# Performance work log

Hardware: AMD Instinct MI355X
Metric: run time of the kernel (lower is better)

The kernel has to match this reference:

```python
import jax, jax.numpy as jnp
import numpy as np

B, S, D, H = 4, 2048, 1024, 16
DEPTH = D // H


def setup_inputs() -> dict:
    key = jax.random.key(0)
    ks = jax.random.split(key, 12)
    q = jax.random.normal(ks[0], (B, S, D), dtype=jnp.float32)
    k = jax.random.normal(ks[1], (B, S, D), dtype=jnp.float32)
    v = jax.random.normal(ks[2], (B, S, D), dtype=jnp.float32)
    # causal mask: 1.0 where attention is disallowed (upper triangle), per `mask * -1e9`
    mask = 1.0 - jnp.tril(jnp.ones((S, S), dtype=jnp.float32))
    mask = mask[None, None, :, :]  # [1,1,S,S] broadcastable over batch/heads
    scale = 1.0 / np.sqrt(D)
    Wq = jax.random.normal(ks[3], (D, D), dtype=jnp.float32) * scale
    Wk = jax.random.normal(ks[4], (D, D), dtype=jnp.float32) * scale
    Wv = jax.random.normal(ks[5], (D, D), dtype=jnp.float32) * scale
    Wo = jax.random.normal(ks[6], (D, D), dtype=jnp.float32) * scale
    bq = jnp.zeros((D,), jnp.float32)
    bk = jnp.zeros((D,), jnp.float32)
    bv = jnp.zeros((D,), jnp.float32)
    bo = jnp.zeros((D,), jnp.float32)
    return {"query": q, "key": k, "value": v, "mask": mask,
            "Wq": Wq, "bq": bq, "Wk": Wk, "bk": bk,
            "Wv": Wv, "bv": bv, "Wo": Wo, "bo": bo}


def _split_heads(x):
    # [B, S, D] -> [B, H, S, depth]
    b, s, _ = x.shape
    return x.reshape(b, s, H, DEPTH).transpose(0, 2, 1, 3)


def reference(query, key, value, mask, Wq, bq, Wk, bk, Wv, bv, Wo, bo):
    q = _split_heads(query @ Wq + bq)   # [B,H,S,depth]
    k = _split_heads(key @ Wk + bk)
    v = _split_heads(value @ Wv + bv)
    scores = jnp.einsum('bhqd,bhkd->bhqk', q, k) / jnp.sqrt(
        jnp.asarray(DEPTH, q.dtype))
    scores = scores + mask * (-1e9)
    attn = jax.nn.softmax(scores, axis=-1)
    out = jnp.einsum('bhqk,bhkd->bhqd', attn, v)   # [B,H,S,depth]
    out = out.transpose(0, 2, 1, 3).reshape(query.shape[0], -1, H * DEPTH)
    return out @ Wo + bo
```

## Files before the change

kernel.cpp:

```cpp
#include <hip/hip_runtime.h>

#define Bsz 4
#define SEQ 2048
#define DIM 1024
#define NH 16
#define HD 64

typedef float  f32x4  __attribute__((ext_vector_type(4)));
typedef __bf16 bf16x8 __attribute__((ext_vector_type(8)));
typedef __bf16 bf16x4 __attribute__((ext_vector_type(4)));
typedef short  s16x4  __attribute__((ext_vector_type(4)));

__device__ __forceinline__ f32x4 mfma16(bf16x8 a, bf16x8 b, f32x4 c) {
    return __builtin_amdgcn_mfma_f32_16x16x32_bf16(a, b, c, 0, 0, 0);
}
__device__ __forceinline__ f32x4 mfma16k16(bf16x4 a, bf16x4 b, f32x4 c) {
#if defined(__has_builtin) && __has_builtin(__builtin_amdgcn_mfma_f32_16x16x16bf16_1k)
    return __builtin_amdgcn_mfma_f32_16x16x16bf16_1k(
        __builtin_bit_cast(s16x4, a), __builtin_bit_cast(s16x4, b), c, 0, 0, 0);
#else
    asm volatile("s_nop 2\n\tv_mfma_f32_16x16x16_bf16 %0, %1, %2, %0\n\ts_nop 7\n\ts_nop 7"
                 : "+v"(c) : "v"(a), "v"(b));
    return c;
#endif
}

#define GLD_LDS16(gsrc, ldst)                                                        \
    __builtin_amdgcn_global_load_lds(                                                \
        (const __attribute__((address_space(1))) void*)(gsrc),                       \
        (__attribute__((address_space(3))) void*)(ldst), 16, 0, 0)

__global__ __launch_bounds__(256) void cvt_kernel(
    const float* __restrict__ x0, const float* __restrict__ x1,
    const float* __restrict__ x2,
    __bf16* __restrict__ o0, __bf16* __restrict__ o1, __bf16* __restrict__ o2)
{
    int z = blockIdx.y;
    const float* X = (z == 0) ? x0 : (z == 1) ? x1 : x2;
    __bf16*      O = (z == 0) ? o0 : (z == 1) ? o1 : o2;
    size_t i = ((size_t)blockIdx.x * 256 + threadIdx.x) * 8;
    f32x4 a = *(const f32x4*)(X + i);
    f32x4 b = *(const f32x4*)(X + i + 4);
    bf16x8 r;
#pragma unroll
    for (int j = 0; j < 4; j++) { r[j] = (__bf16)a[j]; r[4 + j] = (__bf16)b[j]; }
    *(bf16x8*)(O + i) = r;
}

__global__ __launch_bounds__(256) void wt_kernel(
    const float* __restrict__ Wq, const float* __restrict__ Wk,
    const float* __restrict__ Wv, const float* __restrict__ Wo,
    __bf16* __restrict__ wt)
{
    __shared__ float tile[64][65];
    int z = blockIdx.z;
    const float* W = (z == 0) ? Wq : (z == 1) ? Wk : (z == 2) ? Wv : Wo;
    __bf16* out = wt + (size_t)z * DIM * DIM;
    int kb = blockIdx.x * 64, nb = blockIdx.y * 64;
    int t = threadIdx.x;
    int cidx = t & 63, ridx = t >> 6;
#pragma unroll
    for (int i = 0; i < 16; i++) {
        int r = ridx + i * 4;
        tile[r][cidx] = W[(size_t)(kb + r) * DIM + nb + cidx];
    }
    __syncthreads();
#pragma unroll
    for (int i = 0; i < 16; i++) {
        int r = ridx + i * 4;
        out[(size_t)(nb + r) * DIM + kb + cidx] = (__bf16)tile[cidx][r];
    }
}

__global__ __launch_bounds__(256, 2) void gemm_proj(
    const __bf16* __restrict__ Xq, const __bf16* __restrict__ Xk,
    const __bf16* __restrict__ Xv, const __bf16* __restrict__ wt,
    const float* __restrict__ bq, const float* __restrict__ bk,
    const float* __restrict__ bv,
    __bf16* __restrict__ oq, __bf16* __restrict__ ok, __bf16* __restrict__ ovT)
{
    int z = blockIdx.z;
    const __bf16* X    = (z == 0) ? Xq : (z == 1) ? Xk : Xv;
    const float*  bias = (z == 0) ? bq : (z == 1) ? bk : bv;
    const __bf16* Bt   = wt + (size_t)z * DIM * DIM;

    __shared__ __align__(16) char smem[32768];
    __bf16* const Ab = (__bf16*)smem;
    __bf16* const Bb = (__bf16*)(smem + 16384);

    int m0 = blockIdx.x * 128, n0 = blockIdx.y * 128;
    int tid = threadIdx.x, lane = tid & 63, w = tid >> 6;
    int c = lane & 15, g = lane >> 4;
    int wm = (w >> 1) * 64, wn = (w & 1) * 64;

    f32x4 acc[4][4] = {};

    int srow = (w * 2) * 16 + (lane >> 2);
    int scol = (lane & 3) * 8;
    const __bf16* aptr0 = X + (size_t)(m0 + srow) * DIM + scol;
    const __bf16* aptr1 = aptr0 + (size_t)16 * DIM;
    const __bf16* bptr0 = Bt + (size_t)(n0 + srow) * DIM + scol;
    const __bf16* bptr1 = bptr0 + (size_t)16 * DIM;
    int so0 = (w * 2) * 512;
    int so1 = (w * 2 + 1) * 512;

    GLD_LDS16(aptr0, Ab + so0);
    GLD_LDS16(aptr1, Ab + so1);
    GLD_LDS16(bptr0, Bb + so0);
    GLD_LDS16(bptr1, Bb + so1);
    __syncthreads();

    int cur = 0;
    for (int kt = 0; kt < 32; ++kt) {
        int nxt = kt + 1;
        int nb = cur ^ 1;
        if (nxt < 32) {
            int k0 = nxt * 32;
            GLD_LDS16(aptr0 + k0, Ab + nb * 4096 + so0);
            GLD_LDS16(aptr1 + k0, Ab + nb * 4096 + so1);
            GLD_LDS16(bptr0 + k0, Bb + nb * 4096 + so0);
            GLD_LDS16(bptr1 + k0, Bb + nb * 4096 + so1);
        }
        bf16x8 af[4], bf[4];
#pragma unroll
        for (int mf = 0; mf < 4; mf++)
            af[mf] = *(bf16x8*)&Ab[cur * 4096 + (wm + mf * 16 + c) * 32 + g * 8];
#pragma unroll
        for (int nf = 0; nf < 4; nf++)
            bf[nf] = *(bf16x8*)&Bb[cur * 4096 + (wn + nf * 16 + c) * 32 + g * 8];
#pragma unroll
        for (int mf = 0; mf < 4; mf++)
#pragma unroll
            for (int nf = 0; nf < 4; nf++)
                acc[mf][nf] = mfma16(af[mf], bf[nf], acc[mf][nf]);
        __syncthreads();
        cur = nb;
    }

    if (z == 2) {
        __bf16* T = (__bf16*)smem + (size_t)w * 2304;
        int h = (n0 + wn) >> 6;
        int bb = m0 >> 11;
        int s_base = (m0 & (SEQ - 1)) + wm;
        int dd = lane >> 2;
        int ss = (lane & 3) * 8;
        size_t obase = ((size_t)(bb * NH + h) * HD) * SEQ;
#pragma unroll
        for (int half = 0; half < 2; half++) {
#pragma unroll
            for (int mh = 0; mh < 2; mh++) {
                int mf = half * 2 + mh;
#pragma unroll
                for (int nf = 0; nf < 4; nf++) {
                    int col = n0 + wn + nf * 16 + c;
                    int d = nf * 16 + c;
                    float bval = bias[col];
                    bf16x4 pk;
#pragma unroll
                    for (int r = 0; r < 4; r++) pk[r] = (__bf16)(acc[mf][nf][r] + bval);
                    *(bf16x4*)&T[d * 36 + mh * 16 + g * 4] = pk;
                }
            }
#pragma unroll
            for (int dgrp = 0; dgrp < 4; dgrp++) {
                int d = dgrp * 16 + dd;
                bf16x8 vv = *(bf16x8*)&T[d * 36 + ss];
                *(bf16x8*)&ovT[obase + (size_t)d * SEQ + s_base + half * 32 + ss] = vv;
            }
        }
    } else {
        __bf16* Out = (z == 0) ? oq : ok;
#pragma unroll
        for (int nf = 0; nf < 4; nf++) {
            int col = n0 + wn + nf * 16 + c;
            float bval = bias[col];
#pragma unroll
            for (int mf = 0; mf < 4; mf++) {
                int row = m0 + wm + mf * 16 + g * 4;
#pragma unroll
                for (int r = 0; r < 4; r++)
                    Out[(size_t)(row + r) * DIM + col] = (__bf16)(acc[mf][nf][r] + bval);
            }
        }
    }
}

__global__ __launch_bounds__(256, 2) void gemm_proj_f32(
    const float* __restrict__ Xq, const float* __restrict__ Xk,
    const float* __restrict__ Xv, const __bf16* __restrict__ wt,
    const float* __restrict__ bq, const float* __restrict__ bk,
    const float* __restrict__ bv,
    __bf16* __restrict__ oq, __bf16* __restrict__ ok, __bf16* __restrict__ ovT)
{
    int z = blockIdx.z;
    const float*  X    = (z == 0) ? Xq : (z == 1) ? Xk : Xv;
    const float*  bias = (z == 0) ? bq : (z == 1) ? bk : bv;
    const __bf16* Bt   = wt + (size_t)z * DIM * DIM;

    __shared__ __align__(16) char smem[36864];
    __bf16* const Ab = (__bf16*)smem;
    __bf16* const Bb = (__bf16*)(smem + 16384);

    int m0 = blockIdx.x * 128, n0 = blockIdx.y * 128;
    int tid = threadIdx.x, lane = tid & 63, w = tid >> 6;
    int c = lane & 15, g = lane >> 4;
    int wm = (w >> 1) * 64, wn = (w & 1) * 64;

    f32x4 acc[4][4] = {};

    int ar = tid >> 1, ah = tid & 1;
    const float* aptr = X + (size_t)(m0 + ar) * DIM + ah * 16;
    int awo = ar * 32 + ah * 16;

    int brow0 = (w * 2) * 16 + (lane >> 2);
    int bcol  = (lane & 3) * 8;
    const __bf16* bptr0 = Bt + (size_t)(n0 + brow0) * DIM + bcol;
    const __bf16* bptr1 = bptr0 + (size_t)16 * DIM;
    int bwo0 = (w * 2) * 512;
    int bwo1 = (w * 2 + 1) * 512;

    {
        f32x4 f0 = *(const f32x4*)(aptr);
        f32x4 f1 = *(const f32x4*)(aptr + 4);
        f32x4 f2 = *(const f32x4*)(aptr + 8);
        f32x4 f3 = *(const f32x4*)(aptr + 12);
        GLD_LDS16(bptr0, Bb + bwo0);
        GLD_LDS16(bptr1, Bb + bwo1);
        bf16x8 b0, b1;
#pragma unroll
        for (int j = 0; j < 4; j++) {
            b0[j] = (__bf16)f0[j]; b0[4 + j] = (__bf16)f1[j];
            b1[j] = (__bf16)f2[j]; b1[4 + j] = (__bf16)f3[j];
        }
        *(bf16x8*)(Ab + awo)     = b0;
        *(bf16x8*)(Ab + awo + 8) = b1;
    }
    __syncthreads();

    int cur = 0;
    for (int kt = 0; kt < 32; ++kt) {
        int nxt = kt + 1;
        int nb = cur ^ 1;
        f32x4 f0, f1, f2, f3;
        if (nxt < 32) {
            const float* ap = aptr + nxt * 32;
            f0 = *(const f32x4*)(ap);
            f1 = *(const f32x4*)(ap + 4);
            f2 = *(const f32x4*)(ap + 8);
            f3 = *(const f32x4*)(ap + 12);
            GLD_LDS16(bptr0 + nxt * 32, Bb + nb * 4096 + bwo0);
            GLD_LDS16(bptr1 + nxt * 32, Bb + nb * 4096 + bwo1);
        }
        bf16x8 af[4], bf[4];
#pragma unroll
        for (int mf = 0; mf < 4; mf++)
            af[mf] = *(bf16x8*)&Ab[cur * 4096 + (wm + mf * 16 + c) * 32 + g * 8];
#pragma unroll
        for (int nf = 0; nf < 4; nf++)
            bf[nf] = *(bf16x8*)&Bb[cur * 4096 + (wn + nf * 16 + c) * 32 + g * 8];
#pragma unroll
        for (int mf = 0; mf < 4; mf++)
#pragma unroll
            for (int nf = 0; nf < 4; nf++)
                acc[mf][nf] = mfma16(af[mf], bf[nf], acc[mf][nf]);
        if (nxt < 32) {
            bf16x8 b0, b1;
#pragma unroll
            for (int j = 0; j < 4; j++) {
                b0[j] = (__bf16)f0[j]; b0[4 + j] = (__bf16)f1[j];
                b1[j] = (__bf16)f2[j]; b1[4 + j] = (__bf16)f3[j];
            }
            *(bf16x8*)(Ab + nb * 4096 + awo)     = b0;
            *(bf16x8*)(Ab + nb * 4096 + awo + 8) = b1;
        }
        __syncthreads();
        cur = nb;
    }

    if (z == 2) {
        __bf16* T = (__bf16*)smem + (size_t)w * 4608;
#pragma unroll
        for (int nf = 0; nf < 4; nf++) {
            int col = n0 + wn + nf * 16 + c;
            int d = nf * 16 + c;
            float bval = bias[col];
#pragma unroll
            for (int mf = 0; mf < 4; mf++) {
                int sl = mf * 16 + g * 4;
                bf16x4 pk;
#pragma unroll
                for (int r = 0; r < 4; r++) pk[r] = (__bf16)(acc[mf][nf][r] + bval);
                *(bf16x4*)&T[d * 72 + sl] = pk;
            }
        }
        int h = (n0 + wn) >> 6;
        int bb = m0 >> 11;
        int s_base = (m0 & (SEQ - 1)) + wm;
        int dd = lane >> 2;
        int ss = (lane & 3) * 8;
        size_t obase = ((size_t)(bb * NH + h) * HD) * SEQ;
#pragma unroll
        for (int dgrp = 0; dgrp < 4; dgrp++)
#pragma unroll
            for (int half = 0; half < 2; half++) {
                int d = dgrp * 16 + dd;
                int s = half * 32 + ss;
                bf16x8 vv = *(bf16x8*)&T[d * 72 + s];
                *(bf16x8*)&ovT[obase + (size_t)d * SEQ + s_base + s] = vv;
            }
    } else {
        __bf16* Out = (z == 0) ? oq : ok;
#pragma unroll
        for (int nf = 0; nf < 4; nf++) {
            int col = n0 + wn + nf * 16 + c;
            float bval = bias[col];
#pragma unroll
            for (int mf = 0; mf < 4; mf++) {
                int row = m0 + wm + mf * 16 + g * 4;
#pragma unroll
                for (int r = 0; r < 4; r++)
                    Out[(size_t)(row + r) * DIM + col] = (__bf16)(acc[mf][nf][r] + bval);
            }
        }
    }
}

#define QSCALE 0.180336880f

__global__ __launch_bounds__(256, 2) void fa_kernel(
    const __bf16* __restrict__ qp, const __bf16* __restrict__ kp,
    const __bf16* __restrict__ vpT, __bf16* __restrict__ op)
{
    int bz = blockIdx.x;
    int bh = bz & 63;
    int b = bh >> 4, h = bh & 15;
    int qt = 31 - (bz >> 6);
    int q0 = qt * 64;

    int tid = threadIdx.x, lane = tid & 63, w = tid >> 6;
    int c = lane & 15, g = lane >> 4;

    __shared__ __bf16 Kbuf[64 * 64];
    __shared__ __bf16 Vbuf[64 * 64];

    const int qb = q0 + w * 16;
    const int qg = qb + c;

    bf16x8 qf[2];
    {
        const __bf16* qbase = qp + (size_t)(b * SEQ + qg) * DIM + h * HD;
#pragma unroll
        for (int kc = 0; kc < 2; kc++) {
            bf16x8 raw = *(const bf16x8*)(qbase + kc * 32 + g * 8);
            bf16x8 sc;
#pragma unroll
            for (int j = 0; j < 8; j++) sc[j] = (__bf16)((float)raw[j] * QSCALE);
            qf[kc] = sc;
        }
    }

    f32x4 acc[4] = {};
    float m_run = -1e30f;
    float l_run = 0.f;

    int r8 = tid >> 3, c8 = tid & 7;
    int sch = c8 ^ (r8 & 7);
    const __bf16* kbase = kp  + (size_t)(b * SEQ + r8) * DIM + h * HD + sch * 8;
    const __bf16* vbase = vpT + ((size_t)(b * NH + h) * HD + r8) * SEQ + sch * 8;
    __bf16* kdst0 = Kbuf + w * 512;
    __bf16* kdst1 = Kbuf + 2048 + w * 512;
    __bf16* vdst0 = Vbuf + w * 512;
    __bf16* vdst1 = Vbuf + 2048 + w * 512;

    int vb4[4];
#pragma unroll
    for (int mkey = 0; mkey < 4; mkey++)
        vb4[mkey] = c * 64 + (((2 * mkey + (g >> 1)) ^ (c & 7)) * 8) + (g & 1) * 4;

    int ktmax = qt + 1;
    for (int kt = 0; kt < ktmax; ++kt) {
        GLD_LDS16(kbase + (size_t)kt * 64 * DIM, kdst0);
        GLD_LDS16(kbase + (size_t)(kt * 64 + 32) * DIM, kdst1);
        GLD_LDS16(vbase + kt * 64, vdst0);
        GLD_LDS16(vbase + kt * 64 + (size_t)32 * SEQ, vdst1);
        __syncthreads();

        int kb0 = kt * 64;

        f32x4 s[4] = {};
#pragma unroll
        for (int kc = 0; kc < 2; kc++) {
            bf16x8 kf[4];
#pragma unroll
            for (int mkey = 0; mkey < 4; mkey++)
                kf[mkey] = *(bf16x8*)&Kbuf[(mkey * 16 + c) * 64 + (((kc * 4 + g) ^ (c & 7)) * 8)];
#pragma unroll
            for (int mkey = 0; mkey < 4; mkey++)
                s[mkey] = mfma16(kf[mkey], qf[kc], s[mkey]);
        }

        if (kb0 + 63 > qg) {
#pragma unroll
            for (int mkey = 0; mkey < 4; mkey++)
#pragma unroll
                for (int r2 = 0; r2 < 4; r2++)
                    if (kb0 + mkey * 16 + g * 4 + r2 > qg) s[mkey][r2] = -1e30f;
        }

        float pm0 = fmaxf(fmaxf(s[0][0], s[0][1]), fmaxf(s[0][2], s[0][3]));
        float pm1 = fmaxf(fmaxf(s[1][0], s[1][1]), fmaxf(s[1][2], s[1][3]));
        float pm2 = fmaxf(fmaxf(s[2][0], s[2][1]), fmaxf(s[2][2], s[2][3]));
        float pm3 = fmaxf(fmaxf(s[3][0], s[3][1]), fmaxf(s[3][2], s[3][3]));
        float pm = fmaxf(fmaxf(pm0, pm1), fmaxf(pm2, pm3));
        pm = fmaxf(pm, __shfl_xor(pm, 16));
        pm = fmaxf(pm, __shfl_xor(pm, 32));
        if (!__all(pm <= m_run + 8.f)) {
            float mn = fmaxf(m_run, pm);
            float scl = exp2f(m_run - mn);
            l_run *= scl;
#pragma unroll
            for (int nf = 0; nf < 4; nf++) acc[nf] *= scl;
            m_run = mn;
        }
        float rs = 0.f;
        bf16x4 pf[4];
#pragma unroll
        for (int mkey = 0; mkey < 4; mkey++) {
            bf16x4 pk;
#pragma unroll
            for (int r2 = 0; r2 < 4; r2++) {
                float p = exp2f(s[mkey][r2] - m_run);
                rs += p;
                pk[r2] = (__bf16)p;
            }
            pf[mkey] = pk;
        }
        rs += __shfl_xor(rs, 16);
        rs += __shfl_xor(rs, 32);
        l_run += rs;

#pragma unroll
        for (int mkey = 0; mkey < 4; mkey++) {
#pragma unroll
            for (int nf = 0; nf < 4; nf++) {
                bf16x4 vf = *(bf16x4*)&Vbuf[vb4[mkey] + nf * 1024];
                acc[nf] = mfma16k16(vf, pf[mkey], acc[nf]);
            }
        }
        __syncthreads();
    }

    {
        float inv = 1.f / l_run;
        __bf16* obase = op + (size_t)(b * SEQ + qg) * DIM + h * HD + g * 4;
#pragma unroll
        for (int nf = 0; nf < 4; nf++) {
            bf16x4 pk;
#pragma unroll
            for (int r2 = 0; r2 < 4; r2++) pk[r2] = (__bf16)(acc[nf][r2] * inv);
            *(bf16x4*)(obase + nf * 16) = pk;
        }
    }
}

__global__ __launch_bounds__(256, 2) void gemm_out(
    const __bf16* __restrict__ Ain, const __bf16* __restrict__ wt,
    const float* __restrict__ bias, float* __restrict__ Out)
{
    const __bf16* Bt = wt + (size_t)3 * DIM * DIM;

    __shared__ __bf16 Ab[2][4096];
    __shared__ __bf16 Bb[2][4096];

    int m0 = blockIdx.x * 128, n0 = blockIdx.y * 128;
    int tid = threadIdx.x, lane = tid & 63, w = tid >> 6;
    int c = lane & 15, g = lane >> 4;
    int wm = (w >> 1) * 64, wn = (w & 1) * 64;

    f32x4 acc[4][4] = {};

    int srow = (w * 2) * 16 + (lane >> 2);
    int scol = (lane & 3) * 8;
    const __bf16* aptr0 = Ain + (size_t)(m0 + srow) * DIM + scol;
    const __bf16* aptr1 = aptr0 + (size_t)16 * DIM;
    const __bf16* bptr0 = Bt + (size_t)(n0 + srow) * DIM + scol;
    const __bf16* bptr1 = bptr0 + (size_t)16 * DIM;
    int so0 = (w * 2) * 512;
    int so1 = (w * 2 + 1) * 512;

    GLD_LDS16(aptr0, Ab[0] + so0);
    GLD_LDS16(aptr1, Ab[0] + so1);
    GLD_LDS16(bptr0, Bb[0] + so0);
    GLD_LDS16(bptr1, Bb[0] + so1);
    __syncthreads();

    int cur = 0;
    for (int kt = 0; kt < 32; ++kt) {
        int nxt = kt + 1;
        int nb = cur ^ 1;
        if (nxt < 32) {
            int k0 = nxt * 32;
            GLD_LDS16(aptr0 + k0, Ab[nb] + so0);
            GLD_LDS16(aptr1 + k0, Ab[nb] + so1);
            GLD_LDS16(bptr0 + k0, Bb[nb] + so0);
            GLD_LDS16(bptr1 + k0, Bb[nb] + so1);
        }
        bf16x8 af[4], bf[4];
#pragma unroll
        for (int mf = 0; mf < 4; mf++)
            af[mf] = *(bf16x8*)&Ab[cur][(wm + mf * 16 + c) * 32 + g * 8];
#pragma unroll
        for (int nf = 0; nf < 4; nf++)
            bf[nf] = *(bf16x8*)&Bb[cur][(wn + nf * 16 + c) * 32 + g * 8];
#pragma unroll
        for (int mf = 0; mf < 4; mf++)
#pragma unroll
            for (int nf = 0; nf < 4; nf++)
                acc[mf][nf] = mfma16(af[mf], bf[nf], acc[mf][nf]);
        __syncthreads();
        cur = nb;
    }

#pragma unroll
    for (int nf = 0; nf < 4; nf++) {
        int col = n0 + wn + nf * 16 + c;
        float bval = bias[col];
#pragma unroll
        for (int mf = 0; mf < 4; mf++) {
            int row = m0 + wm + mf * 16 + g * 4;
#pragma unroll
            for (int r = 0; r < 4; r++)
                Out[(size_t)(row + r) * DIM + col] = acc[mf][nf][r] + bval;
        }
    }
}

extern "C" void kernel_launch(void* const* d_in, const int* in_sizes, int n_in,
                              void* d_out, int out_size, void* d_ws, size_t ws_size,
                              hipStream_t stream)
{
    const float* q  = (const float*)d_in[0];
    const float* k  = (const float*)d_in[1];
    const float* v  = (const float*)d_in[2];
    const float* Wq = (const float*)d_in[4];
    const float* bq = (const float*)d_in[5];
    const float* Wk = (const float*)d_in[6];
    const float* bk = (const float*)d_in[7];
    const float* Wv = (const float*)d_in[8];
    const float* bv = (const float*)d_in[9];
    const float* Wo = (const float*)d_in[10];
    const float* bo = (const float*)d_in[11];

    char* ws = (char*)d_ws;
    __bf16* wt  = (__bf16*)ws;
    __bf16* qp  = (__bf16*)(ws + (size_t)(8u  << 20));
    __bf16* kp  = (__bf16*)(ws + (size_t)(24u << 20));
    __bf16* vpT = (__bf16*)(ws + (size_t)(40u << 20));
    __bf16* ao  = (__bf16*)(ws + (size_t)(56u << 20));
    __bf16* xq  = (__bf16*)(ws + (size_t)(72u << 20));
    __bf16* xk  = (__bf16*)(ws + (size_t)(88u << 20));
    __bf16* xv  = (__bf16*)(ws + (size_t)(104u << 20));

    wt_kernel<<<dim3(16, 16, 4), 256, 0, stream>>>(Wq, Wk, Wv, Wo, wt);
    if (ws_size >= ((size_t)120u << 20)) {
        cvt_kernel<<<dim3(4096, 3), 256, 0, stream>>>(q, k, v, xq, xk, xv);
        gemm_proj<<<dim3(64, 8, 3), 256, 0, stream>>>(xq, xk, xv, wt, bq, bk, bv, qp, kp, vpT);
    } else {
        gemm_proj_f32<<<dim3(64, 8, 3), 256, 0, stream>>>(q, k, v, wt, bq, bk, bv, qp, kp, vpT);
    }
    fa_kernel<<<dim3(2048), 256, 0, stream>>>(qp, kp, vpT, ao);
    gemm_out<<<dim3(64, 8), 256, 0, stream>>>(ao, wt, bo, (float*)d_out);

    (void)in_sizes; (void)n_in; (void)out_size;
}
```

Before: 196.2 us.

## Double-buffer K/V tiles in LDS and prefetch the next tile during compute

K and V shared-memory buffers are doubled. The next 64-key tile is issued as a global-to-LDS load before the current tile's QK and PV MFMAs run, which drops the top-of-loop barrier that waited on each load. The row-max reduction is rewritten as a linear chain suited to three-input max instructions, and the row-sum is split into four independent accumulators. LDS use per block doubles, which could limit occupancy, and correctness relies on the end-of-loop barrier waiting for the outstanding async loads.

```diff
diff --git a/kernel.cpp b/kernel.cpp
--- a/kernel.cpp
+++ b/kernel.cpp
@@ -340,8 +340,8 @@
     int tid = threadIdx.x, lane = tid & 63, w = tid >> 6;
     int c = lane & 15, g = lane >> 4;
 
-    __shared__ __bf16 Kbuf[64 * 64];
-    __shared__ __bf16 Vbuf[64 * 64];
+    __shared__ __bf16 Kbuf[2 * 64 * 64];
+    __shared__ __bf16 Vbuf[2 * 64 * 64];
 
     const int qb = q0 + w * 16;
     const int qg = qb + c;
@@ -367,10 +367,8 @@
     int sch = c8 ^ (r8 & 7);
     const __bf16* kbase = kp  + (size_t)(b * SEQ + r8) * DIM + h * HD + sch * 8;
     const __bf16* vbase = vpT + ((size_t)(b * NH + h) * HD + r8) * SEQ + sch * 8;
-    __bf16* kdst0 = Kbuf + w * 512;
-    __bf16* kdst1 = Kbuf + 2048 + w * 512;
-    __bf16* vdst0 = Vbuf + w * 512;
-    __bf16* vdst1 = Vbuf + 2048 + w * 512;
+    int sdo0 = w * 512;
+    int sdo1 = 2048 + w * 512;
 
     int vb4[4];
 #pragma unroll
@@ -378,12 +376,22 @@
         vb4[mkey] = c * 64 + (((2 * mkey + (g >> 1)) ^ (c & 7)) * 8) + (g & 1) * 4;
 
     int ktmax = qt + 1;
+
+    GLD_LDS16(kbase,                          Kbuf + sdo0);
+    GLD_LDS16(kbase + (size_t)32 * DIM,       Kbuf + sdo1);
+    GLD_LDS16(vbase,                          Vbuf + sdo0);
+    GLD_LDS16(vbase + (size_t)32 * SEQ,       Vbuf + sdo1);
+    __syncthreads();
+
     for (int kt = 0; kt < ktmax; ++kt) {
-        GLD_LDS16(kbase + (size_t)kt * 64 * DIM, kdst0);
-        GLD_LDS16(kbase + (size_t)(kt * 64 + 32) * DIM, kdst1);
-        GLD_LDS16(vbase + kt * 64, vdst0);
-        GLD_LDS16(vbase + kt * 64 + (size_t)32 * SEQ, vdst1);
-        __syncthreads();
+        int cur = (kt & 1) * 4096;
+        int nb  = ((kt + 1) & 1) * 4096;
+        if (kt + 1 < ktmax) {
+            GLD_LDS16(kbase + (size_t)(kt + 1) * 64 * DIM,        Kbuf + nb + sdo0);
+            GLD_LDS16(kbase + (size_t)((kt + 1) * 64 + 32) * DIM, Kbuf + nb + sdo1);
+            GLD_LDS16(vbase + (kt + 1) * 64,                      Vbuf + nb + sdo0);
+            GLD_LDS16(vbase + (kt + 1) * 64 + (size_t)32 * SEQ,   Vbuf + nb + sdo1);
+        }
 
         int kb0 = kt * 64;
 
@@ -393,7 +401,7 @@
             bf16x8 kf[4];
 #pragma unroll
             for (int mkey = 0; mkey < 4; mkey++)
-                kf[mkey] = *(bf16x8*)&Kbuf[(mkey * 16 + c) * 64 + (((kc * 4 + g) ^ (c & 7)) * 8)];
+                kf[mkey] = *(bf16x8*)&Kbuf[cur + (mkey * 16 + c) * 64 + (((kc * 4 + g) ^ (c & 7)) * 8)];
 #pragma unroll
             for (int mkey = 0; mkey < 4; mkey++)
                 s[mkey] = mfma16(kf[mkey], qf[kc], s[mkey]);
@@ -407,11 +415,14 @@
                     if (kb0 + mkey * 16 + g * 4 + r2 > qg) s[mkey][r2] = -1e30f;
         }
 
-        float pm0 = fmaxf(fmaxf(s[0][0], s[0][1]), fmaxf(s[0][2], s[0][3]));
-        float pm1 = fmaxf(fmaxf(s[1][0], s[1][1]), fmaxf(s[1][2], s[1][3]));
-        float pm2 = fmaxf(fmaxf(s[2][0], s[2][1]), fmaxf(s[2][2], s[2][3]));
-        float pm3 = fmaxf(fmaxf(s[3][0], s[3][1]), fmaxf(s[3][2], s[3][3]));
-        float pm = fmaxf(fmaxf(pm0, pm1), fmaxf(pm2, pm3));
+        float pm = fmaxf(fmaxf(s[0][0], s[0][1]), s[0][2]);
+        pm = fmaxf(fmaxf(pm, s[0][3]), s[1][0]);
+        pm = fmaxf(fmaxf(pm, s[1][1]), s[1][2]);
+        pm = fmaxf(fmaxf(pm, s[1][3]), s[2][0]);
+        pm = fmaxf(fmaxf(pm, s[2][1]), s[2][2]);
+        pm = fmaxf(fmaxf(pm, s[2][3]), s[3][0]);
+        pm = fmaxf(fmaxf(pm, s[3][1]), s[3][2]);
+        pm = fmaxf(pm, s[3][3]);
         pm = fmaxf(pm, __shfl_xor(pm, 16));
         pm = fmaxf(pm, __shfl_xor(pm, 32));
         if (!__all(pm <= m_run + 8.f)) {
@@ -422,7 +433,7 @@
             for (int nf = 0; nf < 4; nf++) acc[nf] *= scl;
             m_run = mn;
         }
-        float rs = 0.f;
+        f32x4 rsv = {0.f, 0.f, 0.f, 0.f};
         bf16x4 pf[4];
 #pragma unroll
         for (int mkey = 0; mkey < 4; mkey++) {
@@ -430,11 +441,12 @@
 #pragma unroll
             for (int r2 = 0; r2 < 4; r2++) {
                 float p = exp2f(s[mkey][r2] - m_run);
-                rs += p;
+                rsv[r2] += p;
                 pk[r2] = (__bf16)p;
             }
             pf[mkey] = pk;
         }
+        float rs = (rsv[0] + rsv[1]) + (rsv[2] + rsv[3]);
         rs += __shfl_xor(rs, 16);
         rs += __shfl_xor(rs, 32);
         l_run += rs;
@@ -443,7 +455,7 @@
         for (int mkey = 0; mkey < 4; mkey++) {
 #pragma unroll
             for (int nf = 0; nf < 4; nf++) {
-                bf16x4 vf = *(bf16x4*)&Vbuf[vb4[mkey] + nf * 1024];
+                bf16x4 vf = *(bf16x4*)&Vbuf[cur + vb4[mkey] + nf * 1024];
                 acc[nf] = mfma16k16(vf, pf[mkey], acc[nf]);
             }
         }
```

Measured after the change: 198.4 us. About the same (+1.1%).
